# Kernel tuning notes

Measured on AMD Instinct MI355X. Metric: run time of the kernel, lower is better.

## Reference

```python
import jax, jax.numpy as jnp
import numpy as np

B, L, D, H = 2, 1024, 512, 8
h = D // H            # head_dim = 64
K = H                 # num_eigh must equal num_heads (vmap pairing in conv)
EPS = 1e-5


def _spectral_filters(seq_len: int, k: int) -> np.ndarray:
    # Hankel matrix Z_{ij} = 2 / ((i+j)^3 - (i+j)), top-k eigenvectors scaled by sigma^{1/4}
    e = np.arange(1, seq_len + 1, dtype=np.float64)
    ipj = e[:, None] + e[None, :]
    Z = 2.0 / (ipj ** 3 - ipj)
    sigma, phi = np.linalg.eigh(Z)
    sigma_k = np.clip(sigma[-k:], 1e-9, None)
    return (phi[:, -k:] * sigma_k ** 0.25).astype(np.float32)  # [L, K]


def setup_inputs() -> dict:
    key = jax.random.key(0)
    ks = jax.random.split(key, 8)
    s = 0.02
    return {
        "x": jax.random.normal(ks[0], (B, L, D), jnp.float32),
        "spectral_basis": jnp.asarray(_spectral_filters(L, K)),       # [L, K]
        "wq_w": jax.random.normal(ks[1], (D, D), jnp.float32) * s,
        "wq_b": jnp.zeros((D,), jnp.float32),
        "wk_w": jax.random.normal(ks[2], (D, D), jnp.float32) * s,
        "wk_b": jnp.zeros((D,), jnp.float32),
        "wv_w": jax.random.normal(ks[3], (D, D), jnp.float32) * s,
        "wv_b": jnp.zeros((D,), jnp.float32),
        "wo_w": jax.random.normal(ks[4], (D, D), jnp.float32) * s,
        "wo_b": jnp.zeros((D,), jnp.float32),
        "wg_w": jax.random.normal(ks[5], (h * h,), jnp.float32) * s,  # Linear(h^2 -> 1)
        "wg_b": jnp.zeros((), jnp.float32),
    }


def _causal_fft_conv(u, filt_f, n):
    # u: [B,H,L,h]; filt_f: precomputed rfft of per-head filters [H, F]
    Uf = jnp.fft.rfft(u, n=n, axis=2)                        # [B,H,F,h]
    y = jnp.fft.irfft(Uf * filt_f[None, :, :, None], n=n, axis=2)
    return y[:, :, :L]                                       # truncate full conv -> causal


def reference(x, spectral_basis, wq_w, wq_b, wk_w, wk_b, wv_w, wv_b,
              wo_w, wo_b, wg_w, wg_b):
    # projections -> [B,H,L,h]
    q = (x @ wq_w + wq_b).reshape(B, L, H, h).transpose(0, 2, 1, 3)
    k = (x @ wk_w + wk_b).reshape(B, L, H, h).transpose(0, 2, 1, 3) * h ** (-0.5)
    v = (x @ wv_w + wv_b).reshape(B, L, H, h).transpose(0, 2, 1, 3)

    n = 2 * L
    filt_f = jnp.fft.rfft(spectral_basis.T, n=n, axis=1)     # [H, F] (one filter per head)
    k_conv = _causal_fft_conv(k, filt_f, n)
    v_conv = _causal_fft_conv(v, filt_f, n)

    # gated outer product Z: [B,H,L,h,h]
    Z = jnp.einsum('bhlm,bhln->bhlmn', v_conv, k_conv)
    gate_logits = Z.reshape(B, H, L, h * h) @ wg_w + wg_b    # [B,H,L]
    gates = jax.nn.relu(gate_logits) ** 2 + EPS
    gated_Z = gates[..., None, None] * Z

    # associative scan (additive) over sequence dim
    cumul_gated_Z = jnp.cumsum(gated_Z, axis=2)              # [B,H,L,h,h]
    cumul_gates = jnp.cumsum(gates, axis=2)                  # [B,H,L]
    attn = cumul_gated_Z / (cumul_gates[..., None, None] + EPS)

    # note: original einsum sums over l (and d) independently of s
    ctxt = jnp.einsum('bhsd,bhlde->bhse', q, attn)           # [B,H,L,h]
    norm = jnp.linalg.norm(ctxt, axis=3, keepdims=True)
    unit = ctxt / jnp.maximum(norm, EPS)                     # F.normalize semantics
    out = unit.transpose(0, 2, 1, 3).reshape(B, L, D)
    return out @ wo_w + wo_b
```

## Files before the change

### kernel.cpp

```cpp
#include <hip/hip_runtime.h>
#include <math.h>


typedef __attribute__((ext_vector_type(8))) short short8;
typedef __attribute__((ext_vector_type(4))) float floatx4;

__device__ __forceinline__ unsigned short f2bf(float f) {
    unsigned int u = __float_as_uint(f);
    unsigned int r = (u + 0x7FFFu + ((u >> 16) & 1u)) >> 16;
    return (unsigned short)r;
}

__global__ __launch_bounds__(256) void k_prep(
    const float* __restrict__ x,
    const float* __restrict__ wq, const float* __restrict__ wk,
    const float* __restrict__ wv, const float* __restrict__ wo,
    const float* __restrict__ sb, const float* __restrict__ wg,
    unsigned short* __restrict__ xb,
    unsigned short* __restrict__ wT, unsigned short* __restrict__ woT,
    unsigned short* __restrict__ TB, unsigned short* __restrict__ wgb)
{
    __shared__ float sf[64][65];
    const int blk = blockIdx.x;
    const int tid = threadIdx.x;

    if (blk < 512) {
        const int gid = blk * 256 + tid;
        const float4* x4 = (const float4*)x;
        float4 a = x4[gid*2], b = x4[gid*2+1];
        uint4 o;
        o.x = f2bf(a.x) | ((unsigned)f2bf(a.y) << 16);
        o.y = f2bf(a.z) | ((unsigned)f2bf(a.w) << 16);
        o.z = f2bf(b.x) | ((unsigned)f2bf(b.y) << 16);
        o.w = f2bf(b.z) | ((unsigned)f2bf(b.w) << 16);
        ((uint4*)xb)[gid] = o;
    } else if (blk < 768) {
        const int t = blk - 512;
        const float* src; unsigned short* dst; int n0, c0, k0;
        if (t < 192) {
            int nt = t >> 3, kt = t & 7;
            n0 = nt * 64; k0 = kt * 64;
            int z = n0 >> 9; c0 = n0 & 511;
            src = (z == 0) ? wq : (z == 1) ? wk : wv;
            dst = wT;
        } else {
            int u = t - 192; int nt = u >> 3, kt = u & 7;
            n0 = nt * 64; c0 = n0; k0 = kt * 64;
            src = wo; dst = woT;
        }
        const int rr = tid >> 4, c4 = tid & 15;
        #pragma unroll
        for (int g = 0; g < 4; ++g) {
            int r = g*16 + rr;
            float4 v = *(const float4*)&src[(size_t)(k0 + r)*512 + c0 + c4*4];
            sf[r][c4*4+0]=v.x; sf[r][c4*4+1]=v.y; sf[r][c4*4+2]=v.z; sf[r][c4*4+3]=v.w;
        }
        __syncthreads();
        #pragma unroll
        for (int g = 0; g < 4; ++g) {
            int c = g*16 + rr;
            int kk = c4*4;
            ushort4 o;
            o.x = f2bf(sf[kk+0][c]); o.y = f2bf(sf[kk+1][c]);
            o.z = f2bf(sf[kk+2][c]); o.w = f2bf(sf[kk+3][c]);
            *(ushort4*)&dst[(size_t)(n0 + c)*512 + k0 + kk] = o;
        }
    } else if (blk < 1024) {
        const int u = blk - 768;
        const int h = u >> 5;
        const int r0 = (u & 31) * 32;
        unsigned short* sbc = (unsigned short*)sf;
        for (int i = tid; i < 1024; i += 256)
            sbc[i] = f2bf(sb[i*8 + h]);
        __syncthreads();
        const int rr = tid >> 3, c0 = (tid & 7) * 128;
        const int t = r0 + rr;
        unsigned short* row = TB + ((size_t)h * 1024 + t) * 1024;
        for (int c = c0; c < c0 + 128; c += 8) {
            unsigned short v[8];
            #pragma unroll
            for (int j = 0; j < 8; ++j) {
                int s = c + j;
                v[j] = (t >= s) ? sbc[t - s] : (unsigned short)0;
            }
            uint4 o;
            o.x = v[0] | ((unsigned)v[1]<<16);
            o.y = v[2] | ((unsigned)v[3]<<16);
            o.z = v[4] | ((unsigned)v[5]<<16);
            o.w = v[6] | ((unsigned)v[7]<<16);
            *(uint4*)&row[c] = o;
        }
    } else {
        const float4* wg4 = (const float4*)wg;
        for (int i = tid; i < 512; i += 256) {
            float4 a = wg4[i*2], b = wg4[i*2+1];
            uint4 o;
            o.x = f2bf(a.x) | ((unsigned)f2bf(a.y) << 16);
            o.y = f2bf(a.z) | ((unsigned)f2bf(a.w) << 16);
            o.z = f2bf(b.x) | ((unsigned)f2bf(b.y) << 16);
            o.w = f2bf(b.z) | ((unsigned)f2bf(b.w) << 16);
            ((uint4*)wgb)[i] = o;
        }
    }
}

__global__ __launch_bounds__(256) void k_qkv_mfma(
    const unsigned short* __restrict__ xb, const unsigned short* __restrict__ wT,
    const float* __restrict__ bq, const float* __restrict__ bk,
    const float* __restrict__ bv,
    float* __restrict__ qo, unsigned short* __restrict__ ub2)
{
    const int tid = threadIdx.x;
    const int lane = tid & 63, wave = tid >> 6;
    const int q = lane >> 4, ln = lane & 15;
    const int wm = wave * 32;
    const int m0 = blockIdx.y * 128;
    const int n0 = blockIdx.x * 64;

    __shared__ unsigned short As[128*72];
    __shared__ unsigned short Bs[64*72];

    floatx4 acc[2][4];
    #pragma unroll
    for (int i = 0; i < 2; ++i)
        #pragma unroll
        for (int j = 0; j < 4; ++j)
            acc[i][j] = (floatx4){0.f, 0.f, 0.f, 0.f};

    const uint4* Ag = (const uint4*)xb;
    const uint4* Bg = (const uint4*)wT;
    for (int k0 = 0; k0 < 512; k0 += 64) {
        #pragma unroll
        for (int s = 0; s < 4; ++s) {
            int idx = s*256 + tid;
            int r = idx >> 3, cp = idx & 7;
            uint4 va = Ag[(size_t)(m0 + r)*64 + (k0 >> 3) + cp];
            *(uint4*)&As[r*72 + cp*8] = va;
        }
        #pragma unroll
        for (int s = 0; s < 2; ++s) {
            int idx = s*256 + tid;
            int r = idx >> 3, cp = idx & 7;
            uint4 vb = Bg[(size_t)(n0 + r)*64 + (k0 >> 3) + cp];
            *(uint4*)&Bs[r*72 + cp*8] = vb;
        }
        __syncthreads();
        short8 af0[2], af1[2], bf0[4], bf1[4];
        #pragma unroll
        for (int i = 0; i < 2; ++i) {
            af0[i] = *(const short8*)&As[(wm + i*16 + ln)*72 + q*8];
            af1[i] = *(const short8*)&As[(wm + i*16 + ln)*72 + 32 + q*8];
        }
        #pragma unroll
        for (int i = 0; i < 4; ++i) {
            bf0[i] = *(const short8*)&Bs[(i*16 + ln)*72 + q*8];
            bf1[i] = *(const short8*)&Bs[(i*16 + ln)*72 + 32 + q*8];
        }
        #pragma unroll
        for (int mi = 0; mi < 2; ++mi)
            #pragma unroll
            for (int ni = 0; ni < 4; ++ni) {
                acc[mi][ni] = __builtin_amdgcn_mfma_f32_16x16x32_bf16(
                    af0[mi], bf0[ni], acc[mi][ni], 0, 0, 0);
                acc[mi][ni] = __builtin_amdgcn_mfma_f32_16x16x32_bf16(
                    af1[mi], bf1[ni], acc[mi][ni], 0, 0, 0);
            }
        __syncthreads();
    }

    const int z = n0 >> 9;
    if (z == 0) {
        #pragma unroll
        for (int mi = 0; mi < 2; ++mi) {
            #pragma unroll
            for (int ni = 0; ni < 4; ++ni) {
                int c = (n0 + ni*16 + ln) & 511;
                int head = c >> 6, dd = c & 63;
                float bb = bq[c];
                #pragma unroll
                for (int reg = 0; reg < 4; ++reg) {
                    int row = m0 + wm + mi*16 + q*4 + reg;
                    int b = row >> 10, l = row & 1023;
                    qo[(size_t)((b*8 + head)*1024 + l)*64 + dd] =
                        acc[mi][ni][reg] + bb;
                }
            }
        }
    } else {
        const float scale = (z == 1) ? 0.125f : 1.0f;
        const float* bias = (z == 1) ? bk : bv;
        unsigned short* dst = ub2 + (size_t)(z-1) * 16 * 64 * 1024;
        #pragma unroll
        for (int mi = 0; mi < 2; ++mi) {
            #pragma unroll
            for (int ni = 0; ni < 4; ++ni) {
                int c = (n0 + ni*16 + ln) & 511;
                int head = c >> 6, dd = c & 63;
                float bb = bias[c];
                int row0 = m0 + wm + mi*16 + q*4;
                int b = row0 >> 10, l0 = row0 & 1023;
                ushort4 o;
                o.x = f2bf((acc[mi][ni][0] + bb) * scale);
                o.y = f2bf((acc[mi][ni][1] + bb) * scale);
                o.z = f2bf((acc[mi][ni][2] + bb) * scale);
                o.w = f2bf((acc[mi][ni][3] + bb) * scale);
                *(ushort4*)&dst[((size_t)((b*8 + head)*64) + dd)*1024 + l0] = o;
            }
        }
    }
}

__global__ __launch_bounds__(256) void k_conv_mfma(
    const unsigned short* __restrict__ TB,
    const unsigned short* __restrict__ ub2,
    float* __restrict__ kc, float* __restrict__ vc,
    unsigned short* __restrict__ kcb)
{
    const int tid = threadIdx.x;
    const int lane = tid & 63, wave = tid >> 6;
    const int q = lane >> 4, ln = lane & 15;
    const int bht = blockIdx.x;
    const int it  = blockIdx.y;
    const int t0  = it * 64;
    const int bh  = bht & 15, h = bh & 7, tensor = bht >> 4;

    __shared__ unsigned short As[64*72];
    __shared__ unsigned short Bs[64*72];

    const uint4* Ag = (const uint4*)TB;
    const uint4* Bg = (const uint4*)ub2;
    const size_t abase = (size_t)h * 131072 + (size_t)t0 * 128;
    const size_t bbase = (size_t)bht * 8192;

    floatx4 acc[4];
    #pragma unroll
    for (int i = 0; i < 4; ++i) acc[i] = (floatx4){0.f,0.f,0.f,0.f};

    const int kend = t0 + 64;
    for (int k0 = 0; k0 < kend; k0 += 64) {
        #pragma unroll
        for (int s = 0; s < 2; ++s) {
            int idx = s*256 + tid;
            int r = idx >> 3, cp = idx & 7;
            uint4 va = Ag[abase + (size_t)r*128 + (k0 >> 3) + cp];
            uint4 vb = Bg[bbase + (size_t)r*128 + (k0 >> 3) + cp];
            *(uint4*)&As[r*72 + cp*8] = va;
            *(uint4*)&Bs[r*72 + cp*8] = vb;
        }
        __syncthreads();
        short8 a0 = *(const short8*)&As[(wave*16 + ln)*72 + q*8];
        short8 a1 = *(const short8*)&As[(wave*16 + ln)*72 + 32 + q*8];
        #pragma unroll
        for (int ni = 0; ni < 4; ++ni) {
            short8 b0 = *(const short8*)&Bs[(ni*16 + ln)*72 + q*8];
            short8 b1 = *(const short8*)&Bs[(ni*16 + ln)*72 + 32 + q*8];
            acc[ni] = __builtin_amdgcn_mfma_f32_16x16x32_bf16(a0, b0, acc[ni], 0, 0, 0);
            acc[ni] = __builtin_amdgcn_mfma_f32_16x16x32_bf16(a1, b1, acc[ni], 0, 0, 0);
        }
        __syncthreads();
    }

    float* dst = (tensor ? vc : kc) + (size_t)bh * 65536;
    #pragma unroll
    for (int ni = 0; ni < 4; ++ni)
        #pragma unroll
        for (int reg = 0; reg < 4; ++reg) {
            int row = t0 + wave*16 + q*4 + reg;
            dst[(size_t)row*64 + ni*16 + ln] = acc[ni][reg];
        }
    if (!tensor) {
        unsigned short* db = kcb + (size_t)bh * 65536;
        #pragma unroll
        for (int ni = 0; ni < 4; ++ni)
            #pragma unroll
            for (int reg = 0; reg < 4; ++reg) {
                int row = t0 + wave*16 + q*4 + reg;
                db[(size_t)row*64 + ni*16 + ln] = f2bf(acc[ni][reg]);
            }
    }
}

__global__ __launch_bounds__(256) void k_gate_mfma(
    const unsigned short* __restrict__ kcb, const float* __restrict__ vc,
    const unsigned short* __restrict__ wgb, const float* __restrict__ wg_b,
    float* __restrict__ gl)
{
    const int tid = threadIdx.x;
    const int lane = tid & 63, wave = tid >> 6;
    const int q = lane >> 4, ln = lane & 15;
    const int l0 = blockIdx.x * 64;
    const int bh = blockIdx.y;

    __shared__ unsigned short As[64*72];
    __shared__ unsigned short Bs[64*72];

    const uint4* Ag = (const uint4*)(kcb + (size_t)bh * 65536);
    const uint4* Bg = (const uint4*)wgb;
    #pragma unroll
    for (int s = 0; s < 2; ++s) {
        int idx = s*256 + tid;
        int r = idx >> 3, cp = idx & 7;
        *(uint4*)&As[r*72 + cp*8] = Ag[(size_t)(l0 + r)*8 + cp];
        *(uint4*)&Bs[r*72 + cp*8] = Bg[r*8 + cp];
    }
    __syncthreads();

    floatx4 T[4];
    #pragma unroll
    for (int mt = 0; mt < 4; ++mt) T[mt] = (floatx4){0.f,0.f,0.f,0.f};
    #pragma unroll
    for (int k0 = 0; k0 < 64; k0 += 32) {
        short8 a = *(const short8*)&As[(wave*16 + ln)*72 + k0 + q*8];
        #pragma unroll
        for (int mt = 0; mt < 4; ++mt) {
            short8 b = *(const short8*)&Bs[(mt*16 + ln)*72 + k0 + q*8];
            T[mt] = __builtin_amdgcn_mfma_f32_16x16x32_bf16(a, b, T[mt], 0, 0, 0);
        }
    }

    const float* vb = vc + (size_t)bh * 65536;
    float part[4] = {0.f, 0.f, 0.f, 0.f};
    #pragma unroll
    for (int mt = 0; mt < 4; ++mt)
        #pragma unroll
        for (int reg = 0; reg < 4; ++reg) {
            int l = l0 + wave*16 + q*4 + reg;
            part[reg] += T[mt][reg] * vb[(size_t)l*64 + mt*16 + ln];
        }
    #pragma unroll
    for (int reg = 0; reg < 4; ++reg) {
        part[reg] += __shfl_xor(part[reg], 1);
        part[reg] += __shfl_xor(part[reg], 2);
        part[reg] += __shfl_xor(part[reg], 4);
        part[reg] += __shfl_xor(part[reg], 8);
    }
    if (ln == 0) {
        const float wgbias = wg_b[0];
        #pragma unroll
        for (int reg = 0; reg < 4; ++reg) {
            int l = l0 + wave*16 + q*4 + reg;
            float s = part[reg] + wgbias;
            float rr = fmaxf(s, 0.0f);
            gl[bh*1024 + l] = rr*rr + 1e-5f;
        }
    }
}

__global__ __launch_bounds__(256) void k_amat(
    const float* __restrict__ kc, const float* __restrict__ vc,
    const float* __restrict__ gl, float* __restrict__ apart)
{
    const int tid = threadIdx.x, tx = tid & 15, ty = tid >> 4;
    const int bh = blockIdx.x, slc = blockIdx.y;
    const float* kb = kc + (size_t)bh * 65536;
    const float* vb = vc + (size_t)bh * 65536;

    __shared__ float sbuf[256];
    __shared__ float wfull[1024];
    __shared__ __align__(16) float vs[16][68];
    __shared__ __align__(16) float ks2[16][68];

    {
        const float4 g4 = ((const float4*)(gl + bh*1024))[tid];
        float g[4] = {g4.x, g4.y, g4.z, g4.w};
        float p[4];
        p[0]=g[0]; p[1]=p[0]+g[1]; p[2]=p[1]+g[2]; p[3]=p[2]+g[3];
        const float s = p[3];
        sbuf[tid] = s;
        __syncthreads();
        for (int off = 1; off < 256; off <<= 1) {
            float t = (tid >= off) ? sbuf[tid-off] : 0.0f;
            __syncthreads();
            sbuf[tid] += t;
            __syncthreads();
        }
        const float base = sbuf[tid] - s;
        float r[4], pr[4];
        #pragma unroll
        for (int u = 0; u < 4; ++u) r[u] = 1.0f / (base + p[u] + 1e-5f);
        pr[0]=r[0]; pr[1]=pr[0]+r[1]; pr[2]=pr[1]+r[2]; pr[3]=pr[2]+r[3];
        const float sr = pr[3];
        __syncthreads();
        sbuf[tid] = sr;
        __syncthreads();
        for (int off = 1; off < 256; off <<= 1) {
            float t = (tid >= off) ? sbuf[tid-off] : 0.0f;
            __syncthreads();
            sbuf[tid] += t;
            __syncthreads();
        }
        const float Rtot  = sbuf[255];
        const float baser = sbuf[tid] - sr;
        wfull[tid*4+0] = g[0] * (Rtot - (baser + pr[0]) + r[0]);
        wfull[tid*4+1] = g[1] * (Rtot - (baser + pr[1]) + r[1]);
        wfull[tid*4+2] = g[2] * (Rtot - (baser + pr[2]) + r[2]);
        wfull[tid*4+3] = g[3] * (Rtot - (baser + pr[3]) + r[3]);
    }
    __syncthreads();

    float acc[4][4] = {};
    const float4* k4 = (const float4*)kb;
    const float4* v4 = (const float4*)vb;
    for (int j0 = slc*128; j0 < slc*128 + 128; j0 += 16) {
        {
            int r = tid >> 4, c4 = tid & 15;
            *(float4*)&vs[r][c4*4]  = v4[(size_t)(j0 + r)*16 + c4];
            *(float4*)&ks2[r][c4*4] = k4[(size_t)(j0 + r)*16 + c4];
        }
        __syncthreads();
        #pragma unroll
        for (int jj = 0; jj < 16; ++jj) {
            float wj = wfull[j0 + jj];
            float a[4];
            a[0] = vs[jj][ty*4+0]*wj; a[1] = vs[jj][ty*4+1]*wj;
            a[2] = vs[jj][ty*4+2]*wj; a[3] = vs[jj][ty*4+3]*wj;
            float4 b4 = *(const float4*)&ks2[jj][tx*4];
            float bb[4] = {b4.x, b4.y, b4.z, b4.w};
            #pragma unroll
            for (int ii = 0; ii < 4; ++ii)
                #pragma unroll
                for (int jc = 0; jc < 4; ++jc)
                    acc[ii][jc] += a[ii] * bb[jc];
        }
        __syncthreads();
    }
    float* ap = apart + (size_t)(slc*16 + bh) * 4096;
    #pragma unroll
    for (int i = 0; i < 4; ++i) {
        float4 o = { acc[i][0], acc[i][1], acc[i][2], acc[i][3] };
        *(float4*)&ap[(ty*4+i)*64 + tx*4] = o;
    }
}

__global__ __launch_bounds__(256) void k_ctxt(
    const float* __restrict__ q, const float* __restrict__ apart,
    unsigned short* __restrict__ ub)
{
    const int tid = threadIdx.x, tx = tid & 15, ty = tid >> 4;
    const int l0 = blockIdx.x * 64;
    const int bh = blockIdx.y;
    const float* qb = q + (size_t)bh * 65536;

    __shared__ __align__(16) float qs[64][20];
    __shared__ __align__(16) float As[16][68];
    float acc[4][4] = {};
    const float4* q4 = (const float4*)qb;
    const float4* a4 = (const float4*)apart;
    for (int d0 = 0; d0 < 64; d0 += 16) {
        {
            int r = tid >> 2, c4 = tid & 3;
            float4 t = q4[(size_t)(l0 + r)*16 + (d0 >> 2) + c4];
            *(float4*)&qs[r][c4*4] = t;
        }
        {
            int r = tid >> 4, c4 = tid & 15;
            size_t o = (size_t)(d0 + r)*16 + c4;
            float4 t = a4[(size_t)(0*16 + bh)*1024 + o];
            #pragma unroll
            for (int s = 1; s < 8; ++s) {
                float4 u = a4[(size_t)(s*16 + bh)*1024 + o];
                t.x += u.x; t.y += u.y; t.z += u.z; t.w += u.w;
            }
            *(float4*)&As[r][c4*4] = t;
        }
        __syncthreads();
        float qreg[4][16];
        #pragma unroll
        for (int i = 0; i < 4; ++i)
            #pragma unroll
            for (int c = 0; c < 4; ++c) {
                float4 t = *(const float4*)&qs[ty*4+i][c*4];
                qreg[i][c*4+0] = t.x; qreg[i][c*4+1] = t.y;
                qreg[i][c*4+2] = t.z; qreg[i][c*4+3] = t.w;
            }
        #pragma unroll
        for (int dd = 0; dd < 16; ++dd) {
            float4 b4 = *(const float4*)&As[dd][tx*4];
            float bb[4] = {b4.x, b4.y, b4.z, b4.w};
            #pragma unroll
            for (int ii = 0; ii < 4; ++ii)
                #pragma unroll
                for (int jj = 0; jj < 4; ++jj)
                    acc[ii][jj] += qreg[ii][dd] * bb[jj];
        }
        __syncthreads();
    }
    __shared__ float red[64][17];
    __shared__ float nrm[64];
    #pragma unroll
    for (int i = 0; i < 4; ++i) {
        red[ty*4+i][tx] = acc[i][0]*acc[i][0] + acc[i][1]*acc[i][1]
                        + acc[i][2]*acc[i][2] + acc[i][3]*acc[i][3];
    }
    __syncthreads();
    if (tid < 64) {
        float s = 0.0f;
        #pragma unroll
        for (int t = 0; t < 16; ++t) s += red[tid][t];
        nrm[tid] = fmaxf(sqrtf(s), 1e-5f);
    }
    __syncthreads();
    const int b = bh >> 3, hd = bh & 7;
    #pragma unroll
    for (int i = 0; i < 4; ++i) {
        int lr = ty*4 + i;
        float inv = 1.0f / nrm[lr];
        ushort4 o;
        o.x = f2bf(acc[i][0]*inv); o.y = f2bf(acc[i][1]*inv);
        o.z = f2bf(acc[i][2]*inv); o.w = f2bf(acc[i][3]*inv);
        *(ushort4*)&ub[(size_t)(b*1024 + l0 + lr)*512 + hd*64 + tx*4] = o;
    }
}

__global__ __launch_bounds__(256) void k_out_mfma(
    const unsigned short* __restrict__ ub, const unsigned short* __restrict__ woT,
    const float* __restrict__ bo, float* __restrict__ out)
{
    const int tid = threadIdx.x;
    const int lane = tid & 63, wave = tid >> 6;
    const int q = lane >> 4, ln = lane & 15;
    const int wm = wave * 32;
    const int m0 = blockIdx.y * 128;
    const int n0 = blockIdx.x * 64;

    __shared__ unsigned short As[128*72];
    __shared__ unsigned short Bs[64*72];

    floatx4 acc[2][4];
    #pragma unroll
    for (int i = 0; i < 2; ++i)
        #pragma unroll
        for (int j = 0; j < 4; ++j)
            acc[i][j] = (floatx4){0.f, 0.f, 0.f, 0.f};

    const uint4* Ag = (const uint4*)ub;
    const uint4* Bg = (const uint4*)woT;
    for (int k0 = 0; k0 < 512; k0 += 64) {
        #pragma unroll
        for (int s = 0; s < 4; ++s) {
            int idx = s*256 + tid;
            int r = idx >> 3, cp = idx & 7;
            uint4 va = Ag[(size_t)(m0 + r)*64 + (k0 >> 3) + cp];
            *(uint4*)&As[r*72 + cp*8] = va;
        }
        #pragma unroll
        for (int s = 0; s < 2; ++s) {
            int idx = s*256 + tid;
            int r = idx >> 3, cp = idx & 7;
            uint4 vb = Bg[(size_t)(n0 + r)*64 + (k0 >> 3) + cp];
            *(uint4*)&Bs[r*72 + cp*8] = vb;
        }
        __syncthreads();
        short8 af0[2], af1[2], bf0[4], bf1[4];
        #pragma unroll
        for (int i = 0; i < 2; ++i) {
            af0[i] = *(const short8*)&As[(wm + i*16 + ln)*72 + q*8];
            af1[i] = *(const short8*)&As[(wm + i*16 + ln)*72 + 32 + q*8];
        }
        #pragma unroll
        for (int i = 0; i < 4; ++i) {
            bf0[i] = *(const short8*)&Bs[(i*16 + ln)*72 + q*8];
            bf1[i] = *(const short8*)&Bs[(i*16 + ln)*72 + 32 + q*8];
        }
        #pragma unroll
        for (int mi = 0; mi < 2; ++mi)
            #pragma unroll
            for (int ni = 0; ni < 4; ++ni) {
                acc[mi][ni] = __builtin_amdgcn_mfma_f32_16x16x32_bf16(
                    af0[mi], bf0[ni], acc[mi][ni], 0, 0, 0);
                acc[mi][ni] = __builtin_amdgcn_mfma_f32_16x16x32_bf16(
                    af1[mi], bf1[ni], acc[mi][ni], 0, 0, 0);
            }
        __syncthreads();
    }

    #pragma unroll
    for (int mi = 0; mi < 2; ++mi) {
        #pragma unroll
        for (int ni = 0; ni < 4; ++ni) {
            int gcol = n0 + ni*16 + ln;
            float bb = bo[gcol];
            #pragma unroll
            for (int reg = 0; reg < 4; ++reg) {
                int row = m0 + wm + mi*16 + q*4 + reg;
                out[(size_t)row*512 + gcol] = acc[mi][ni][reg] + bb;
            }
        }
    }
}

extern "C" void kernel_launch(void* const* d_in, const int* in_sizes, int n_in,
                              void* d_out, int out_size, void* d_ws, size_t ws_size,
                              hipStream_t stream)
{
    const float* x   = (const float*)d_in[0];
    const float* sb  = (const float*)d_in[1];
    const float* wq  = (const float*)d_in[2];
    const float* bq  = (const float*)d_in[3];
    const float* wk  = (const float*)d_in[4];
    const float* bk  = (const float*)d_in[5];
    const float* wv  = (const float*)d_in[6];
    const float* bv  = (const float*)d_in[7];
    const float* wo  = (const float*)d_in[8];
    const float* bo  = (const float*)d_in[9];
    const float* wg  = (const float*)d_in[10];
    const float* wgb = (const float*)d_in[11];
    float* out = (float*)d_out;
    float* ws  = (float*)d_ws;

    float* Q   = ws;
    float* KC  = ws + 1048576;
    float* VC  = ws + 2*1048576;
    float* GL  = ws + 3*1048576;
    float* AP  = GL + 16384;
    float* fp  = AP + 524288;
    unsigned short* XB  = (unsigned short*)fp;
    unsigned short* WT  = XB  + 1048576;
    unsigned short* WOT = WT  + 786432;
    unsigned short* UB  = WOT + 262144;
    unsigned short* UB2 = UB  + 1048576;
    unsigned short* TB  = UB2 + 2097152;
    unsigned short* WGB = TB  + 8388608;
    unsigned short* KCB = WGB + 4096;

    k_prep     <<<dim3(1025),   256, 0, stream>>>(x, wq, wk, wv, wo, sb, wg,
                                                  XB, WT, WOT, TB, WGB);
    k_qkv_mfma <<<dim3(24, 16), 256, 0, stream>>>(XB, WT, bq, bk, bv, Q, UB2);
    k_conv_mfma<<<dim3(32, 16), 256, 0, stream>>>(TB, UB2, KC, VC, KCB);
    k_gate_mfma<<<dim3(16, 16), 256, 0, stream>>>(KCB, VC, WGB, wgb, GL);
    k_amat     <<<dim3(16, 8),  256, 0, stream>>>(KC, VC, GL, AP);
    k_ctxt     <<<dim3(16, 16), 256, 0, stream>>>(Q, AP, UB);
    k_out_mfma <<<dim3(8, 16),  256, 0, stream>>>(UB, WOT, bo, out);
}
```

Baseline: 152.2 us.

## Build Toeplitz filter operand on the fly from reversed filter in LDS

Drops the materialised 8x1024x1024 bf16 Toeplitz matrix that k_prep wrote and k_conv_mfma read back from global memory. Each conv block now loads its head's filter reversed and zero-padded into a small LDS array and assembles the A fragments for the MFMA from shifted windows of it. This removes about 16 MB of global writes and the repeated Toeplitz reads. The cost is per-element scalar LDS reads (unaligned, 8 per fragment) in place of vector loads, plus an sb gather in every block.

```diff
diff --git a/kernel.cpp b/kernel.cpp
--- a/kernel.cpp
+++ b/kernel.cpp
@@ -15,10 +15,10 @@
     const float* __restrict__ x,
     const float* __restrict__ wq, const float* __restrict__ wk,
     const float* __restrict__ wv, const float* __restrict__ wo,
-    const float* __restrict__ sb, const float* __restrict__ wg,
+    const float* __restrict__ wg,
     unsigned short* __restrict__ xb,
     unsigned short* __restrict__ wT, unsigned short* __restrict__ woT,
-    unsigned short* __restrict__ TB, unsigned short* __restrict__ wgb)
+    unsigned short* __restrict__ wgb)
 {
     __shared__ float sf[64][65];
     const int blk = blockIdx.x;
@@ -65,31 +65,6 @@
             o.z = f2bf(sf[kk+2][c]); o.w = f2bf(sf[kk+3][c]);
             *(ushort4*)&dst[(size_t)(n0 + c)*512 + k0 + kk] = o;
         }
-    } else if (blk < 1024) {
-        const int u = blk - 768;
-        const int h = u >> 5;
-        const int r0 = (u & 31) * 32;
-        unsigned short* sbc = (unsigned short*)sf;
-        for (int i = tid; i < 1024; i += 256)
-            sbc[i] = f2bf(sb[i*8 + h]);
-        __syncthreads();
-        const int rr = tid >> 3, c0 = (tid & 7) * 128;
-        const int t = r0 + rr;
-        unsigned short* row = TB + ((size_t)h * 1024 + t) * 1024;
-        for (int c = c0; c < c0 + 128; c += 8) {
-            unsigned short v[8];
-            #pragma unroll
-            for (int j = 0; j < 8; ++j) {
-                int s = c + j;
-                v[j] = (t >= s) ? sbc[t - s] : (unsigned short)0;
-            }
-            uint4 o;
-            o.x = v[0] | ((unsigned)v[1]<<16);
-            o.y = v[2] | ((unsigned)v[3]<<16);
-            o.z = v[4] | ((unsigned)v[5]<<16);
-            o.w = v[6] | ((unsigned)v[7]<<16);
-            *(uint4*)&row[c] = o;
-        }
     } else {
         const float4* wg4 = (const float4*)wg;
         for (int i = tid; i < 512; i += 256) {
@@ -211,7 +186,7 @@
 }
 
 __global__ __launch_bounds__(256) void k_conv_mfma(
-    const unsigned short* __restrict__ TB,
+    const float* __restrict__ sb,
     const unsigned short* __restrict__ ub2,
     float* __restrict__ kc, float* __restrict__ vc,
     unsigned short* __restrict__ kcb)
@@ -224,12 +199,15 @@
     const int t0  = it * 64;
     const int bh  = bht & 15, h = bh & 7, tensor = bht >> 4;
 
-    __shared__ unsigned short As[64*72];
+    __shared__ unsigned short revf[1152];
     __shared__ unsigned short Bs[64*72];
 
-    const uint4* Ag = (const uint4*)TB;
+    for (int i = tid; i < 1152; i += 256) {
+        int d = 1087 - i;
+        revf[i] = (d >= 0 && d < 1024) ? f2bf(sb[d*8 + h]) : (unsigned short)0;
+    }
+
     const uint4* Bg = (const uint4*)ub2;
-    const size_t abase = (size_t)h * 131072 + (size_t)t0 * 128;
     const size_t bbase = (size_t)bht * 8192;
 
     floatx4 acc[4];
@@ -237,19 +215,23 @@
     for (int i = 0; i < 4; ++i) acc[i] = (floatx4){0.f,0.f,0.f,0.f};
 
     const int kend = t0 + 64;
+    const int arow = 1087 - t0 - (wave*16 + ln);
     for (int k0 = 0; k0 < kend; k0 += 64) {
         #pragma unroll
         for (int s = 0; s < 2; ++s) {
             int idx = s*256 + tid;
             int r = idx >> 3, cp = idx & 7;
-            uint4 va = Ag[abase + (size_t)r*128 + (k0 >> 3) + cp];
             uint4 vb = Bg[bbase + (size_t)r*128 + (k0 >> 3) + cp];
-            *(uint4*)&As[r*72 + cp*8] = va;
             *(uint4*)&Bs[r*72 + cp*8] = vb;
         }
         __syncthreads();
-        short8 a0 = *(const short8*)&As[(wave*16 + ln)*72 + q*8];
-        short8 a1 = *(const short8*)&As[(wave*16 + ln)*72 + 32 + q*8];
+        const int ab = arow + k0 + q*8;
+        short8 a0, a1;
+        #pragma unroll
+        for (int j = 0; j < 8; ++j) {
+            a0[j] = (short)revf[ab + j];
+            a1[j] = (short)revf[ab + 32 + j];
+        }
         #pragma unroll
         for (int ni = 0; ni < 4; ++ni) {
             short8 b0 = *(const short8*)&Bs[(ni*16 + ln)*72 + q*8];
@@ -619,14 +601,13 @@
     unsigned short* WOT = WT  + 786432;
     unsigned short* UB  = WOT + 262144;
     unsigned short* UB2 = UB  + 1048576;
-    unsigned short* TB  = UB2 + 2097152;
-    unsigned short* WGB = TB  + 8388608;
+    unsigned short* WGB = UB2 + 2097152;
     unsigned short* KCB = WGB + 4096;
 
-    k_prep     <<<dim3(1025),   256, 0, stream>>>(x, wq, wk, wv, wo, sb, wg,
-                                                  XB, WT, WOT, TB, WGB);
+    k_prep     <<<dim3(769),    256, 0, stream>>>(x, wq, wk, wv, wo, wg,
+                                                  XB, WT, WOT, WGB);
     k_qkv_mfma <<<dim3(24, 16), 256, 0, stream>>>(XB, WT, bq, bk, bv, Q, UB2);
-    k_conv_mfma<<<dim3(32, 16), 256, 0, stream>>>(TB, UB2, KC, VC, KCB);
+    k_conv_mfma<<<dim3(32, 16), 256, 0, stream>>>(sb, UB2, KC, VC, KCB);
     k_gate_mfma<<<dim3(16, 16), 256, 0, stream>>>(KCB, VC, WGB, wgb, GL);
     k_amat     <<<dim3(16, 8),  256, 0, stream>>>(KC, VC, GL, AP);
     k_ctxt     <<<dim3(16, 16), 256, 0, stream>>>(Q, AP, UB);
```

New measurement: 148.8 us (median of 2 runs). -2.3%, faster.
